# Performance work log

Measured on AMD Instinct MI355X. Metric: run time of the kernel, lower is better.

The kernel has to match this reference:

```python
import jax, jax.numpy as jnp
import numpy as np

COMMITMENT_COST = 0.25


def setup_inputs() -> dict:
    key = jax.random.key(0)
    k1, k2 = jax.random.split(key)
    z_e = jax.random.normal(k1, (32, 256, 32, 32), dtype=jnp.float32)
    codebook = jax.random.normal(k2, (1024, 256), dtype=jnp.float32)
    return {"z_e": z_e, "codebook": codebook}


def reference(z_e, codebook):
    B, D, H, W = z_e.shape
    # (B, D, H, W) -> (N, D), N = B*H*W
    z_flat = jnp.transpose(z_e, (0, 2, 3, 1)).reshape(-1, D)
    # squared L2 distances to every codebook entry: (N, K)
    distances = (
        jnp.sum(z_flat * z_flat, axis=1, keepdims=True)
        - 2.0 * (z_flat @ codebook.T)
        + jnp.sum(codebook * codebook, axis=1)
    )
    codes = jnp.argmin(distances, axis=1)          # (N,)
    z_q = jnp.transpose(codebook[codes].reshape(B, H, W, D), (0, 3, 1, 2))
    # straight-through estimator
    z_q_st = z_e + jax.lax.stop_gradient(z_q - z_e)
    codebook_loss = jnp.mean((jax.lax.stop_gradient(z_q) - z_e) ** 2)
    commitment_loss = jnp.mean((z_q - jax.lax.stop_gradient(z_e)) ** 2)
    vq_loss = codebook_loss + COMMITMENT_COST * commitment_loss
    indices = codes.reshape(B, H, W)
    return z_q_st, indices, vq_loss
```

## Files before the change

### kernel.cpp

```cpp
#include <hip/hip_runtime.h>
#include <cstdint>
#include <cstddef>


typedef __attribute__((ext_vector_type(8))) short bf16x8;
typedef __attribute__((ext_vector_type(4))) float f32x4;

#define GL2LDS(g, l) __builtin_amdgcn_global_load_lds( \
    (__attribute__((address_space(1))) const void*)(g), \
    (__attribute__((address_space(3))) void*)(l), 16, 0, 0)

__device__ __forceinline__ unsigned short rne_bf16(float f) {
    unsigned u = __float_as_uint(f);
    return (unsigned short)((u + 0x7FFFu + ((u >> 16) & 1u)) >> 16);
}
__device__ __forceinline__ float bf16_to_f(unsigned short h) {
    return __uint_as_float((unsigned)h << 16);
}

__global__ __launch_bounds__(256)
void vq_cnorm_kernel(const float* __restrict__ cb, float* __restrict__ cnorm)
{
    const int k = blockIdx.x * 256 + threadIdx.x;
    const float4* row = reinterpret_cast<const float4*>(cb + (size_t)k * 256);
    float s0 = 0.f, s1 = 0.f, s2 = 0.f, s3 = 0.f;
#pragma unroll 8
    for (int i = 0; i < 64; ++i) {
        float4 v = row[i];
        s0 = fmaf(v.x, v.x, s0);
        s1 = fmaf(v.y, v.y, s1);
        s2 = fmaf(v.z, v.z, s2);
        s3 = fmaf(v.w, v.w, s3);
    }
    cnorm[k] = (s0 + s1) + (s2 + s3);
}

__global__ __launch_bounds__(256)
void vq_csplit_kernel(const float* __restrict__ cb, unsigned short* __restrict__ c0,
                      unsigned short* __restrict__ c1, unsigned short* __restrict__ c2)
{
    const int idx = blockIdx.x * 256 + threadIdx.x;
    float4 v = reinterpret_cast<const float4*>(cb)[idx];
    float f[4] = { v.x, v.y, v.z, v.w };
    ushort4 h0, h1, h2;
    unsigned short* p0[4] = { &h0.x, &h0.y, &h0.z, &h0.w };
    unsigned short* p1[4] = { &h1.x, &h1.y, &h1.z, &h1.w };
    unsigned short* p2[4] = { &h2.x, &h2.y, &h2.z, &h2.w };
#pragma unroll
    for (int j = 0; j < 4; ++j) {
        unsigned short b0 = rne_bf16(f[j]); float r1 = f[j] - bf16_to_f(b0);
        unsigned short b1 = rne_bf16(r1);   float r2 = r1 - bf16_to_f(b1);
        unsigned short b2 = rne_bf16(r2);
        *p0[j] = b0; *p1[j] = b1; *p2[j] = b2;
    }
    reinterpret_cast<ushort4*>(c0)[idx] = h0;
    reinterpret_cast<ushort4*>(c1)[idx] = h1;
    reinterpret_cast<ushort4*>(c2)[idx] = h2;
}

__global__ __launch_bounds__(256)
void vq_zsplit_kernel(const float* __restrict__ z, unsigned short* __restrict__ z0,
                      unsigned short* __restrict__ z1, unsigned short* __restrict__ z2)
{
    __shared__ float zl[64 * 264];
    const int t = threadIdx.x, blk = blockIdx.x;
    const int b = blk >> 4, hw0 = (blk & 15) << 6;
    const float* zb = z + ((size_t)b << 18) + hw0;
#pragma unroll 8
    for (int i = 0; i < 64; ++i) {
        int idx = i * 256 + t;
        int d = idx >> 6, hwl = idx & 63;
        zl[hwl * 264 + d] = zb[(size_t)d * 1024 + hwl];
    }
    __syncthreads();
    const int n0 = (b << 10) + hw0;
#pragma unroll
    for (int p = 0; p < 8; ++p) {
        const int hwl = p * 8 + (t >> 5);
        const int d0 = (t & 31) * 8;
        const float* src = &zl[hwl * 264 + d0];
        unsigned short h0[8], h1[8], h2[8];
#pragma unroll
        for (int j = 0; j < 8; ++j) {
            float f = src[j];
            unsigned short b0 = rne_bf16(f);  float r1 = f - bf16_to_f(b0);
            unsigned short b1 = rne_bf16(r1); float r2 = r1 - bf16_to_f(b1);
            unsigned short b2 = rne_bf16(r2);
            h0[j] = b0; h1[j] = b1; h2[j] = b2;
        }
        const size_t o = (size_t)(n0 + hwl) * 256 + d0;
        ushort4 a;
        a = ushort4{h0[0],h0[1],h0[2],h0[3]}; *reinterpret_cast<ushort4*>(z0 + o)     = a;
        a = ushort4{h0[4],h0[5],h0[6],h0[7]}; *reinterpret_cast<ushort4*>(z0 + o + 4) = a;
        a = ushort4{h1[0],h1[1],h1[2],h1[3]}; *reinterpret_cast<ushort4*>(z1 + o)     = a;
        a = ushort4{h1[4],h1[5],h1[6],h1[7]}; *reinterpret_cast<ushort4*>(z1 + o + 4) = a;
        a = ushort4{h2[0],h2[1],h2[2],h2[3]}; *reinterpret_cast<ushort4*>(z2 + o)     = a;
        a = ushort4{h2[4],h2[5],h2[6],h2[7]}; *reinterpret_cast<ushort4*>(z2 + o + 4) = a;
    }
}

__global__ __launch_bounds__(256)
void vq_mfma_argmin_kernel(const unsigned short* __restrict__ zp,
                           const unsigned short* __restrict__ cp,
                           const float* __restrict__ cnorm,
                           unsigned long long* __restrict__ packed)
{
    __shared__ unsigned short At[2][128 * 64];
    __shared__ unsigned short Bt[2][128 * 64];

    const int t = threadIdx.x, l = t & 63, w = t >> 6;
    const int wr = w >> 1, wc = w & 1;
    const int nid = ((blockIdx.x & 7) << 8) | (blockIdx.x >> 3);
    const int bm = nid >> 3, bn = nid & 7;
    const int arow = bm * 128, brow = bn * 128;

    f32x4 acc[4][4];
#pragma unroll
    for (int m = 0; m < 4; ++m)
#pragma unroll
        for (int n = 0; n < 4; ++n) acc[m][n] = f32x4{0.f, 0.f, 0.f, 0.f};

    const int srow = w * 8 + (l >> 3);
    const int scol = (((l & 7) ^ ((l >> 3) & 7))) * 8;

    const int lo16 = l & 15, hi4 = l >> 4, l7 = l & 7;
    const int coff0 = ((hi4    ) ^ l7) * 8;
    const int coff1 = ((hi4 + 4) ^ l7) * 8;

    const int ASEG[6] = { 0, 1, 2, 0, 1, 0 };
    const int BSEG[6] = { 0, 0, 0, 1, 1, 2 };

#define VQ_STAGE(ss, bb) do {                                                 \
    const unsigned short* As_ = zp + (size_t)ASEG[(ss) >> 2] * 8388608u;      \
    const unsigned short* Bs_ = cp + (size_t)BSEG[(ss) >> 2] * 262144u;       \
    const int ko_ = ((ss) & 3) << 6;                                          \
    _Pragma("unroll")                                                         \
    for (int i = 0; i < 4; ++i) {                                             \
        GL2LDS(As_ + (size_t)(arow + i * 32 + srow) * 256 + ko_ + scol,       \
               &At[bb][(i * 32 + w * 8) * 64]);                               \
        GL2LDS(Bs_ + (size_t)(brow + i * 32 + srow) * 256 + ko_ + scol,       \
               &Bt[bb][(i * 32 + w * 8) * 64]);                               \
    }                                                                         \
} while (0)

    VQ_STAGE(0, 0);
    __syncthreads();

#pragma unroll
    for (int s = 0; s < 24; ++s) {
        const int cur = s & 1;
        if (s < 23) VQ_STAGE(s + 1, cur ^ 1);
        __builtin_amdgcn_sched_barrier(0);

#pragma unroll
        for (int kk = 0; kk < 2; ++kk) {
            const int co = kk ? coff1 : coff0;
            bf16x8 a[4], b[4];
#pragma unroll
            for (int m = 0; m < 4; ++m)
                a[m] = *reinterpret_cast<const bf16x8*>(
                    &At[cur][(wr * 64 + m * 16 + lo16) * 64 + co]);
#pragma unroll
            for (int n = 0; n < 4; ++n)
                b[n] = *reinterpret_cast<const bf16x8*>(
                    &Bt[cur][(wc * 64 + n * 16 + lo16) * 64 + co]);
#pragma unroll
            for (int m = 0; m < 4; ++m)
#pragma unroll
                for (int n = 0; n < 4; ++n)
                    acc[m][n] = __builtin_amdgcn_mfma_f32_16x16x32_bf16(
                        a[m], b[n], acc[m][n], 0, 0, 0);
        }
        if (s < 23) __syncthreads();
    }
#undef VQ_STAGE

    int coln[4]; float cnv[4];
#pragma unroll
    for (int n = 0; n < 4; ++n) {
        coln[n] = brow + wc * 64 + n * 16 + lo16;
        cnv[n] = cnorm[coln[n]];
    }
#pragma unroll
    for (int m = 0; m < 4; ++m) {
#pragma unroll
        for (int j = 0; j < 4; ++j) {
            unsigned long long best = 0xFFFFFFFFFFFFFFFFull;
#pragma unroll
            for (int n = 0; n < 4; ++n) {
                float d = fmaf(-2.0f, acc[m][n][j], cnv[n]);
                unsigned u = __float_as_uint(d);
                u = (u & 0x80000000u) ? ~u : (u | 0x80000000u);
                unsigned long long pk = ((unsigned long long)u << 32) | (unsigned)coln[n];
                best = pk < best ? pk : best;
            }
#pragma unroll
            for (int mask = 1; mask <= 8; mask <<= 1) {
                unsigned long long o = __shfl_xor(best, mask, 64);
                best = o < best ? o : best;
            }
            if (lo16 == 0) {
                const int row = arow + wr * 64 + m * 16 + hi4 * 4 + j;
                atomicMin(&packed[row], best);
            }
        }
    }
}

__global__ __launch_bounds__(256, 2)
void vq_gather_packed_kernel(const float* __restrict__ cb, const float* __restrict__ z,
                             const unsigned long long* __restrict__ packed,
                             float* __restrict__ out_zq, float* __restrict__ out_idx,
                             float* __restrict__ loss)
{
    __shared__ float rows[64 * 257];
    __shared__ int   ks[64];
    __shared__ float wsum[4];

    const int t   = threadIdx.x;
    const int blk = blockIdx.x;
    const int b   = blk >> 4;
    const int hw0 = (blk & 15) << 6;
    const int n0  = blk << 6;

    if (t < 64) {
        const int k = (int)(packed[n0 + t] & 0xFFFFFFFFull);
        ks[t] = k;
        out_idx[n0 + t] = (float)k;
    }
    __syncthreads();

#pragma unroll 4
    for (int i = 0; i < 64; ++i) {
        rows[i * 257 + t] = cb[(size_t)ks[i] * 256 + t];
    }
    __syncthreads();

    const int dq = t >> 6;
    const int hw = t & 63;
    const size_t obase = ((size_t)b << 18) + hw0 + hw;
    float sum = 0.f;
#pragma unroll 4
    for (int dd = 0; dd < 64; ++dd) {
        const int d = (dq << 6) + dd;
        const float  q  = rows[hw * 257 + d];
        const size_t a  = obase + (size_t)d * 1024;
        const float  zv = z[a];
        out_zq[a] = q;
        const float diff = q - zv;
        sum = fmaf(diff, diff, sum);
    }
#pragma unroll
    for (int m = 1; m <= 32; m <<= 1) sum += __shfl_xor(sum, m, 64);
    if ((t & 63) == 0) wsum[t >> 6] = sum;
    __syncthreads();
    if (t == 0) {
        const float s = (wsum[0] + wsum[1]) + (wsum[2] + wsum[3]);
        atomicAdd(loss, s * (1.25f / 8388608.0f));
    }
}

__global__ __launch_bounds__(256)
void vq_transpose_kernel(const float* __restrict__ cb, float* __restrict__ ctT)
{
    __shared__ float tile[64 * 65];
    const int t  = threadIdx.x;
    const int kb = blockIdx.x >> 2, db = blockIdx.x & 3;
    const int k0 = kb << 6, d0 = db << 6;
#pragma unroll
    for (int i = 0; i < 16; ++i) {
        int idx = i * 256 + t;
        int r = idx >> 6, c = idx & 63;
        tile[r * 65 + c] = cb[(size_t)(k0 + r) * 256 + d0 + c];
    }
    __syncthreads();
#pragma unroll
    for (int i = 0; i < 16; ++i) {
        int idx = i * 256 + t;
        int r = idx >> 6, c = idx & 63;
        ctT[(size_t)(d0 + r) * 1024 + k0 + c] = tile[c * 65 + r];
    }
}

__global__ __launch_bounds__(512, 2)
void vq_argmin_kernel(const float* __restrict__ z, const float* __restrict__ ctT,
                      const float* __restrict__ cnorm, int* __restrict__ codes,
                      float* __restrict__ out_idx)
{
    __shared__ float zt[256 * 64];
    __shared__ float ct[16 * 256];
    const int t = threadIdx.x, tx = t & 63, ty = t >> 6, p0 = ty << 3;
    const int blk = blockIdx.x, b = blk >> 4, hw0 = (blk & 15) << 6;
    const float* zbase = z + ((size_t)b << 18) + hw0;
#pragma unroll
    for (int i = 0; i < 8; ++i) {
        int idx = i * 512 + t;
        int d = idx >> 4, c4 = (idx & 15) << 2;
        float4 v = *reinterpret_cast<const float4*>(zbase + (size_t)d * 1024 + c4);
        *reinterpret_cast<float4*>(&zt[d * 64 + c4]) = v;
    }
    float minv[8]; int mini[8];
#pragma unroll
    for (int i = 0; i < 8; ++i) { minv[i] = 3.0e38f; mini[i] = 0; }
    const float* zrd = &zt[p0];
    const float* crd = &ct[tx << 2];
    for (int kt = 0; kt < 4; ++kt) {
        const int k0 = kt << 8;
        float acc[8][4];
#pragma unroll
        for (int i = 0; i < 8; ++i)
#pragma unroll
            for (int j = 0; j < 4; ++j) acc[i][j] = 0.f;
        for (int dc = 0; dc < 16; ++dc) {
            const int d0 = dc << 4;
            __syncthreads();
#pragma unroll
            for (int i = 0; i < 2; ++i) {
                int idx = i * 512 + t;
                int r = idx >> 6, c4 = (idx & 63) << 2;
                float4 v = *reinterpret_cast<const float4*>(ctT + (size_t)(d0 + r) * 1024 + k0 + c4);
                *reinterpret_cast<float4*>(&ct[r * 256 + c4]) = v;
            }
            __syncthreads();
            const float* zp = zrd + d0 * 64;
#pragma unroll
            for (int d = 0; d < 16; ++d) {
                float4 za = *reinterpret_cast<const float4*>(zp + d * 64);
                float4 zb = *reinterpret_cast<const float4*>(zp + d * 64 + 4);
                float4 cc = *reinterpret_cast<const float4*>(crd + d * 256);
#define VQ_FMA_ROW(ii, zv)                          \
                acc[ii][0] = fmaf(zv, cc.x, acc[ii][0]); \
                acc[ii][1] = fmaf(zv, cc.y, acc[ii][1]); \
                acc[ii][2] = fmaf(zv, cc.z, acc[ii][2]); \
                acc[ii][3] = fmaf(zv, cc.w, acc[ii][3]);
                VQ_FMA_ROW(0, za.x) VQ_FMA_ROW(1, za.y) VQ_FMA_ROW(2, za.z) VQ_FMA_ROW(3, za.w)
                VQ_FMA_ROW(4, zb.x) VQ_FMA_ROW(5, zb.y) VQ_FMA_ROW(6, zb.z) VQ_FMA_ROW(7, zb.w)
#undef VQ_FMA_ROW
            }
        }
#pragma unroll
        for (int j = 0; j < 4; ++j) {
            const int k = k0 + (tx << 2) + j;
            const float cn = cnorm[k];
#pragma unroll
            for (int i = 0; i < 8; ++i) {
                float dist = fmaf(-2.0f, acc[i][j], cn);
                if (dist < minv[i]) { minv[i] = dist; mini[i] = k; }
            }
        }
    }
#pragma unroll
    for (int m = 1; m <= 32; m <<= 1) {
#pragma unroll
        for (int i = 0; i < 8; ++i) {
            float ov = __shfl_xor(minv[i], m, 64);
            int   oi = __shfl_xor(mini[i], m, 64);
            if (ov < minv[i] || (ov == minv[i] && oi < mini[i])) { minv[i] = ov; mini[i] = oi; }
        }
    }
    if (tx == 0) {
        const int n0 = (blk << 6) + p0;
#pragma unroll
        for (int i = 0; i < 8; ++i) {
            codes[n0 + i]   = mini[i];
            out_idx[n0 + i] = (float)mini[i];
        }
    }
}

__global__ __launch_bounds__(256, 2)
void vq_gather_kernel(const float* __restrict__ cb, const float* __restrict__ z,
                      const int* __restrict__ codes, float* __restrict__ out_zq,
                      float* __restrict__ loss)
{
    __shared__ float rows[64 * 257];
    __shared__ int   ks[64];
    __shared__ float wsum[4];
    const int t = threadIdx.x, blk = blockIdx.x;
    const int b = blk >> 4, hw0 = (blk & 15) << 6, n0 = blk << 6;
    if (t < 64) ks[t] = codes[n0 + t];
    __syncthreads();
#pragma unroll 4
    for (int i = 0; i < 64; ++i) rows[i * 257 + t] = cb[(size_t)ks[i] * 256 + t];
    __syncthreads();
    const int dq = t >> 6, hw = t & 63;
    const size_t obase = ((size_t)b << 18) + hw0 + hw;
    float sum = 0.f;
#pragma unroll 4
    for (int dd = 0; dd < 64; ++dd) {
        const int d = (dq << 6) + dd;
        const float  q  = rows[hw * 257 + d];
        const size_t a  = obase + (size_t)d * 1024;
        const float  zv = z[a];
        out_zq[a] = q;
        const float diff = q - zv;
        sum = fmaf(diff, diff, sum);
    }
#pragma unroll
    for (int m = 1; m <= 32; m <<= 1) sum += __shfl_xor(sum, m, 64);
    if ((t & 63) == 0) wsum[t >> 6] = sum;
    __syncthreads();
    if (t == 0) {
        const float s = (wsum[0] + wsum[1]) + (wsum[2] + wsum[3]);
        atomicAdd(loss, s * (1.25f / 8388608.0f));
    }
}

extern "C" void kernel_launch(void* const* d_in, const int* in_sizes, int n_in,
                              void* d_out, int out_size, void* d_ws, size_t ws_size,
                              hipStream_t stream)
{
    (void)in_sizes; (void)n_in; (void)out_size;

    const float* z  = (const float*)d_in[0];
    const float* cb = (const float*)d_in[1];

    float* out      = (float*)d_out;
    float* out_zq   = out;
    float* out_idx  = out + 8388608;
    float* out_loss = out + 8421376;

    const size_t NEED = 262144ull + 3ull * 16777216ull + 3ull * 524288ull + 4096ull;

    if (ws_size >= NEED) {
        unsigned long long* packed = (unsigned long long*)d_ws;
        unsigned short* z0 = (unsigned short*)((char*)d_ws + 262144);
        unsigned short* z1 = z0 + 8388608u;
        unsigned short* z2 = z1 + 8388608u;
        unsigned short* c0 = z2 + 8388608u;
        unsigned short* c1 = c0 + 262144u;
        unsigned short* c2 = c1 + 262144u;
        float* cnorm = (float*)(c2 + 262144u);

        hipMemsetAsync(out_loss, 0, sizeof(float), stream);
        hipMemsetAsync(packed, 0xFF, 262144, stream);
        vq_csplit_kernel<<<256, 256, 0, stream>>>(cb, c0, c1, c2);
        vq_cnorm_kernel<<<4, 256, 0, stream>>>(cb, cnorm);
        vq_zsplit_kernel<<<512, 256, 0, stream>>>(z, z0, z1, z2);
        vq_mfma_argmin_kernel<<<2048, 256, 0, stream>>>(z0, c0, cnorm, packed);
        vq_gather_packed_kernel<<<512, 256, 0, stream>>>(cb, z, packed, out_zq, out_idx, out_loss);
    } else {
        float* ctT   = (float*)d_ws;
        float* cnorm = ctT + 256 * 1024;
        int*   codes = (int*)(cnorm + 1024);

        hipMemsetAsync(out_loss, 0, sizeof(float), stream);
        vq_transpose_kernel<<<64, 256, 0, stream>>>(cb, ctT);
        vq_cnorm_kernel<<<4, 256, 0, stream>>>(cb, cnorm);
        vq_argmin_kernel<<<512, 512, 0, stream>>>(z, ctT, cnorm, codes, out_idx);
        vq_gather_kernel<<<512, 256, 0, stream>>>(cb, z, codes, out_zq, out_loss);
    }
}
```

Before: 186.4 us.

## Enlarge MFMA argmin tile to 256x256 with 8 waves and deeper async pipeline

Result: faster. 159.7 us (-14.3%).

```diff
diff --git a/kernel.cpp b/kernel.cpp
--- a/kernel.cpp
+++ b/kernel.cpp
@@ -99,81 +99,116 @@
     }
 }
 
-__global__ __launch_bounds__(256)
+__global__ __launch_bounds__(512, 2)
 void vq_mfma_argmin_kernel(const unsigned short* __restrict__ zp,
                            const unsigned short* __restrict__ cp,
                            const float* __restrict__ cnorm,
                            unsigned long long* __restrict__ packed)
 {
-    __shared__ unsigned short At[2][128 * 64];
-    __shared__ unsigned short Bt[2][128 * 64];
-
-    const int t = threadIdx.x, l = t & 63, w = t >> 6;
-    const int wr = w >> 1, wc = w & 1;
-    const int nid = ((blockIdx.x & 7) << 8) | (blockIdx.x >> 3);
-    const int bm = nid >> 3, bn = nid & 7;
-    const int arow = bm * 128, brow = bn * 128;
-
-    f32x4 acc[4][4];
-#pragma unroll
-    for (int m = 0; m < 4; ++m)
+    __shared__ unsigned short Ld[2][2][2][256 * 32];
+
+    const int tid = threadIdx.x, l = tid & 63, w = tid >> 6;
+    const int wr = w >> 2, wc = w & 3;
+    const int nid = ((blockIdx.x & 7) << 6) | (blockIdx.x >> 3);
+    const int bm = nid >> 2, bn = nid & 3;
+    const int arow = bm * 256, brow = bn * 256;
+
+    f32x4 acc[8][4];
+#pragma unroll
+    for (int m = 0; m < 8; ++m)
 #pragma unroll
         for (int n = 0; n < 4; ++n) acc[m][n] = f32x4{0.f, 0.f, 0.f, 0.f};
 
-    const int srow = w * 8 + (l >> 3);
-    const int scol = (((l & 7) ^ ((l >> 3) & 7))) * 8;
-
-    const int lo16 = l & 15, hi4 = l >> 4, l7 = l & 7;
-    const int coff0 = ((hi4    ) ^ l7) * 8;
-    const int coff1 = ((hi4 + 4) ^ l7) * 8;
-
-    const int ASEG[6] = { 0, 1, 2, 0, 1, 0 };
-    const int BSEG[6] = { 0, 0, 0, 1, 1, 2 };
-
-#define VQ_STAGE(ss, bb) do {                                                 \
-    const unsigned short* As_ = zp + (size_t)ASEG[(ss) >> 2] * 8388608u;      \
-    const unsigned short* Bs_ = cp + (size_t)BSEG[(ss) >> 2] * 262144u;       \
-    const int ko_ = ((ss) & 3) << 6;                                          \
-    _Pragma("unroll")                                                         \
-    for (int i = 0; i < 4; ++i) {                                             \
-        GL2LDS(As_ + (size_t)(arow + i * 32 + srow) * 256 + ko_ + scol,       \
-               &At[bb][(i * 32 + w * 8) * 64]);                               \
-        GL2LDS(Bs_ + (size_t)(brow + i * 32 + srow) * 256 + ko_ + scol,       \
-               &Bt[bb][(i * 32 + w * 8) * 64]);                               \
+    const int srow  = l >> 2;
+    const int selem = (((l & 3) ^ ((l >> 2) & 3))) << 3;
+
+    const int lo16 = l & 15, hi4 = l >> 4;
+    const int fco = ((hi4 ^ (lo16 & 3))) << 3;
+
+#define STAGE(tt, mat, kk) do {                                               \
+    const int seg_ = (tt) >> 2;                                               \
+    const unsigned short* S_ = (mat)                                          \
+        ? cp + (size_t)((0x211000 >> (seg_ << 2)) & 3) * 262144u              \
+        : zp + (size_t)((0x010210 >> (seg_ << 2)) & 3) * 8388608u;            \
+    const int R_  = (mat) ? brow : arow;                                      \
+    const int KO_ = (((tt) & 3) << 6) + ((kk) << 5) + selem;                  \
+    GL2LDS(S_ + (size_t)(R_ + (w * 2 + 0) * 16 + srow) * 256 + KO_,           \
+           &Ld[(tt) & 1][mat][kk][(w * 2 + 0) * 512]);                        \
+    GL2LDS(S_ + (size_t)(R_ + (w * 2 + 1) * 16 + srow) * 256 + KO_,           \
+           &Ld[(tt) & 1][mat][kk][(w * 2 + 1) * 512]);                        \
+} while (0)
+
+#define VM12 asm volatile("s_waitcnt vmcnt(12)" ::: "memory")
+#define VM8  asm volatile("s_waitcnt vmcnt(8)"  ::: "memory")
+#define VM4  asm volatile("s_waitcnt vmcnt(4)"  ::: "memory")
+#define VM0  asm volatile("s_waitcnt vmcnt(0)"  ::: "memory")
+#define NOPS ((void)0)
+#define SBAR do { asm volatile("" ::: "memory");                              \
+                  __builtin_amdgcn_s_barrier();                               \
+                  __builtin_amdgcn_sched_barrier(0); } while (0)
+
+    bf16x8 bfr0, bfr1, bfr2, bfr3;
+
+#define PH(t, mh, kk, STAGESTMT, VMSTMT) do {                                 \
+    const unsigned short* Ap_ = &Ld[(t) & 1][0][kk][0];                       \
+    const unsigned short* Bp_ = &Ld[(t) & 1][1][kk][0];                       \
+    bf16x8 a0, a1, a2, a3;                                                    \
+    a0 = *(const bf16x8*)&Ap_[(wr*128 + ((mh)*4+0)*16 + lo16)*32 + fco];      \
+    a1 = *(const bf16x8*)&Ap_[(wr*128 + ((mh)*4+1)*16 + lo16)*32 + fco];      \
+    a2 = *(const bf16x8*)&Ap_[(wr*128 + ((mh)*4+2)*16 + lo16)*32 + fco];      \
+    a3 = *(const bf16x8*)&Ap_[(wr*128 + ((mh)*4+3)*16 + lo16)*32 + fco];      \
+    if ((mh) == 0) {                                                          \
+        bfr0 = *(const bf16x8*)&Bp_[(wc*64 + 0*16 + lo16)*32 + fco];          \
+        bfr1 = *(const bf16x8*)&Bp_[(wc*64 + 1*16 + lo16)*32 + fco];          \
+        bfr2 = *(const bf16x8*)&Bp_[(wc*64 + 2*16 + lo16)*32 + fco];          \
+        bfr3 = *(const bf16x8*)&Bp_[(wc*64 + 3*16 + lo16)*32 + fco];          \
     }                                                                         \
+    STAGESTMT;                                                                \
+    SBAR;                                                                     \
+    __builtin_amdgcn_s_setprio(1);                                            \
+    acc[(mh)*4+0][0] = __builtin_amdgcn_mfma_f32_16x16x32_bf16(a0, bfr0, acc[(mh)*4+0][0], 0,0,0); \
+    acc[(mh)*4+0][1] = __builtin_amdgcn_mfma_f32_16x16x32_bf16(a0, bfr1, acc[(mh)*4+0][1], 0,0,0); \
+    acc[(mh)*4+0][2] = __builtin_amdgcn_mfma_f32_16x16x32_bf16(a0, bfr2, acc[(mh)*4+0][2], 0,0,0); \
+    acc[(mh)*4+0][3] = __builtin_amdgcn_mfma_f32_16x16x32_bf16(a0, bfr3, acc[(mh)*4+0][3], 0,0,0); \
+    acc[(mh)*4+1][0] = __builtin_amdgcn_mfma_f32_16x16x32_bf16(a1, bfr0, acc[(mh)*4+1][0], 0,0,0); \
+    acc[(mh)*4+1][1] = __builtin_amdgcn_mfma_f32_16x16x32_bf16(a1, bfr1, acc[(mh)*4+1][1], 0,0,0); \
+    acc[(mh)*4+1][2] = __builtin_amdgcn_mfma_f32_16x16x32_bf16(a1, bfr2, acc[(mh)*4+1][2], 0,0,0); \
+    acc[(mh)*4+1][3] = __builtin_amdgcn_mfma_f32_16x16x32_bf16(a1, bfr3, acc[(mh)*4+1][3], 0,0,0); \
+    acc[(mh)*4+2][0] = __builtin_amdgcn_mfma_f32_16x16x32_bf16(a2, bfr0, acc[(mh)*4+2][0], 0,0,0); \
+    acc[(mh)*4+2][1] = __builtin_amdgcn_mfma_f32_16x16x32_bf16(a2, bfr1, acc[(mh)*4+2][1], 0,0,0); \
+    acc[(mh)*4+2][2] = __builtin_amdgcn_mfma_f32_16x16x32_bf16(a2, bfr2, acc[(mh)*4+2][2], 0,0,0); \
+    acc[(mh)*4+2][3] = __builtin_amdgcn_mfma_f32_16x16x32_bf16(a2, bfr3, acc[(mh)*4+2][3], 0,0,0); \
+    acc[(mh)*4+3][0] = __builtin_amdgcn_mfma_f32_16x16x32_bf16(a3, bfr0, acc[(mh)*4+3][0], 0,0,0); \
+    acc[(mh)*4+3][1] = __builtin_amdgcn_mfma_f32_16x16x32_bf16(a3, bfr1, acc[(mh)*4+3][1], 0,0,0); \
+    acc[(mh)*4+3][2] = __builtin_amdgcn_mfma_f32_16x16x32_bf16(a3, bfr2, acc[(mh)*4+3][2], 0,0,0); \
+    acc[(mh)*4+3][3] = __builtin_amdgcn_mfma_f32_16x16x32_bf16(a3, bfr3, acc[(mh)*4+3][3], 0,0,0); \
+    __builtin_amdgcn_s_setprio(0);                                            \
+    VMSTMT;                                                                   \
+    SBAR;                                                                     \
 } while (0)
 
-    VQ_STAGE(0, 0);
-    __syncthreads();
-
-#pragma unroll
-    for (int s = 0; s < 24; ++s) {
-        const int cur = s & 1;
-        if (s < 23) VQ_STAGE(s + 1, cur ^ 1);
-        __builtin_amdgcn_sched_barrier(0);
-
-#pragma unroll
-        for (int kk = 0; kk < 2; ++kk) {
-            const int co = kk ? coff1 : coff0;
-            bf16x8 a[4], b[4];
-#pragma unroll
-            for (int m = 0; m < 4; ++m)
-                a[m] = *reinterpret_cast<const bf16x8*>(
-                    &At[cur][(wr * 64 + m * 16 + lo16) * 64 + co]);
-#pragma unroll
-            for (int n = 0; n < 4; ++n)
-                b[n] = *reinterpret_cast<const bf16x8*>(
-                    &Bt[cur][(wc * 64 + n * 16 + lo16) * 64 + co]);
-#pragma unroll
-            for (int m = 0; m < 4; ++m)
-#pragma unroll
-                for (int n = 0; n < 4; ++n)
-                    acc[m][n] = __builtin_amdgcn_mfma_f32_16x16x32_bf16(
-                        a[m], b[n], acc[m][n], 0, 0, 0);
-        }
-        if (s < 23) __syncthreads();
-    }
-#undef VQ_STAGE
+#define TILE(t, SA0, SB0, SA1, SB1, V2, V4)                                   \
+    PH(t, 0, 0, SA0, NOPS);                                                   \
+    PH(t, 1, 0, SB0, V2);                                                     \
+    PH(t, 0, 1, SA1, NOPS);                                                   \
+    PH(t, 1, 1, SB1, V4)
+
+    STAGE(0, 0, 0); STAGE(0, 1, 0); STAGE(0, 0, 1); STAGE(0, 1, 1);
+    STAGE(1, 0, 0); STAGE(1, 1, 0); STAGE(1, 0, 1); STAGE(1, 1, 1);
+    VM12;
+    SBAR;
+
+    TILE(0, NOPS, NOPS, NOPS, NOPS, VM8, VM4);
+#pragma unroll 2
+    for (int t = 1; t <= 22; ++t) {
+        TILE(t, STAGE(t + 1, 0, 0), STAGE(t + 1, 1, 0),
+                STAGE(t + 1, 0, 1), STAGE(t + 1, 1, 1), VM4, VM4);
+    }
+    TILE(23, NOPS, NOPS, NOPS, NOPS, VM0, NOPS);
+
+#undef TILE
+#undef PH
+#undef STAGE
 
     int coln[4]; float cnv[4];
 #pragma unroll
@@ -182,7 +217,7 @@
         cnv[n] = cnorm[coln[n]];
     }
 #pragma unroll
-    for (int m = 0; m < 4; ++m) {
+    for (int m = 0; m < 8; ++m) {
 #pragma unroll
         for (int j = 0; j < 4; ++j) {
             unsigned long long best = 0xFFFFFFFFFFFFFFFFull;
@@ -200,7 +235,7 @@
                 best = o < best ? o : best;
             }
             if (lo16 == 0) {
-                const int row = arow + wr * 64 + m * 16 + hi4 * 4 + j;
+                const int row = arow + wr * 128 + m * 16 + hi4 * 4 + j;
                 atomicMin(&packed[row], best);
             }
         }
@@ -437,7 +472,7 @@
         vq_csplit_kernel<<<256, 256, 0, stream>>>(cb, c0, c1, c2);
         vq_cnorm_kernel<<<4, 256, 0, stream>>>(cb, cnorm);
         vq_zsplit_kernel<<<512, 256, 0, stream>>>(z, z0, z1, z2);
-        vq_mfma_argmin_kernel<<<2048, 256, 0, stream>>>(z0, c0, cnorm, packed);
+        vq_mfma_argmin_kernel<<<512, 512, 0, stream>>>(z0, c0, cnorm, packed);
         vq_gather_packed_kernel<<<512, 256, 0, stream>>>(cb, z, packed, out_zq, out_idx, out_loss);
     } else {
         float* ctT   = (float*)d_ws;
```
